# Performance work log

Hardware: AMD Instinct MI355X
Metric: run time of the kernel (lower is better)

The kernel has to match this reference:

```python
import jax, jax.numpy as jnp
import numpy as np

N_OUT = 100_000   # destination (output) nodes
N_IN = 200_000    # source nodes (x_feat rows); first N_OUT are the self/dst nodes
DEG = 16          # sample_count / fixed fan-out
E = N_OUT * DEG   # edges
D_IN = 128
D_OUT = 128


def setup_inputs() -> dict:
    key = jax.random.key(0)
    k1, k2, k3 = jax.random.split(key, 3)
    x_feat = jax.random.normal(k1, (N_IN, D_IN), dtype=jnp.float32)
    # MFG CSR with fixed fan-out DEG (what make_mfg_csr(sample_size=DEG) encodes)
    csr_row_ptr = jnp.arange(N_OUT + 1, dtype=jnp.int64) * DEG
    csr_col_ind = jax.random.randint(k2, (E,), 0, N_IN, dtype=jnp.int64)
    # Linear(2*D_IN, D_OUT) with xavier_uniform(gain for relu) weight
    gain = float(np.sqrt(2.0))
    fan_in, fan_out = 2 * D_IN, D_OUT
    bound = gain * float(np.sqrt(6.0 / (fan_in + fan_out)))
    W = jax.random.uniform(k3, (D_OUT, 2 * D_IN), dtype=jnp.float32,
                           minval=-bound, maxval=bound)
    lin_bias = jnp.zeros((D_OUT,), dtype=jnp.float32)
    bias = jnp.zeros((D_OUT,), dtype=jnp.float32)  # extra additive Parameter
    return {"x_feat": x_feat, "csr_row_ptr": csr_row_ptr,
            "csr_col_ind": csr_col_ind, "sample_count": DEG,
            "W": W, "lin_bias": lin_bias, "bias": bias}


def _segment_ids(row_ptr, n_edges):
    # seg[e] = destination row of edge e; handles empty rows via duplicate adds
    ones = jnp.zeros((n_edges,), dtype=jnp.int32).at[row_ptr[1:-1]].add(1)
    return jnp.cumsum(ones)


def reference(x_feat, csr_row_ptr, csr_col_ind, sample_count, W, lin_bias, bias):
    n_out = csr_row_ptr.shape[0] - 1
    n_edges = csr_col_ind.shape[0]
    seg = _segment_ids(csr_row_ptr, n_edges)
    # mean aggregation over sampled neighbors (cugraphops agg 'mean')
    gathered = x_feat[csr_col_ind]                          # [E, D_IN]
    summed = jax.ops.segment_sum(gathered, seg, num_segments=n_out)
    deg = (csr_row_ptr[1:] - csr_row_ptr[:-1]).astype(x_feat.dtype)
    mean_agg = summed / jnp.maximum(deg, 1.0)[:, None]      # [n_out, D_IN]
    # concat self (dst) features with aggregated features, then Linear
    x_agg = jnp.concatenate([x_feat[:n_out], mean_agg], axis=-1)  # [n_out, 2*D_IN]
    y = x_agg @ W.T + lin_bias + bias
    return y
```

## Files before the change

kernel.cpp:

```cpp
#include <hip/hip_runtime.h>
#include <hip/hip_bf16.h>

#define D 128
#define K2 256
#define NT 64
#define NTHREADS 256
#define AGM_LD 136
#define WT_LD 68

typedef __attribute__((ext_vector_type(8))) short bf16x8;
typedef __attribute__((ext_vector_type(4))) float f32x4;
typedef __attribute__((ext_vector_type(2))) float f32x2;

static __device__ __forceinline__ unsigned short f2bf(float f) {
    __hip_bfloat16 h = __float2bfloat16(f);
    return *reinterpret_cast<unsigned short*>(&h);
}

static __device__ __forceinline__ unsigned int f2q_manual(float f) {
    f = fminf(fmaxf(f, -448.f), 448.f);
    unsigned int u = __float_as_uint(f * 0x1.0p-120f);
    const unsigned int lsb = (u >> 20) & 1u;
    u += 0x7ffffu + lsb;
    return ((u >> 24) & 0x80u) | ((u >> 20) & 0x7fu);
}
static __device__ __forceinline__ float q2f_manual(unsigned int b) {
    const unsigned int bits = ((b & 0x80u) << 24) | ((b & 0x7fu) << 20);
    return __uint_as_float(bits) * 0x1.0p+120f;
}
static __device__ __forceinline__ unsigned int pack_fp8x4(float4 v) {
#if __has_builtin(__builtin_amdgcn_cvt_pk_fp8_f32)
    int lo = __builtin_amdgcn_cvt_pk_fp8_f32(v.x, v.y, 0, false);
    int q  = __builtin_amdgcn_cvt_pk_fp8_f32(v.z, v.w, lo, true);
    return (unsigned int)q;
#else
    return f2q_manual(v.x) | (f2q_manual(v.y) << 8) |
           (f2q_manual(v.z) << 16) | (f2q_manual(v.w) << 24);
#endif
}
static __device__ __forceinline__ f32x2 unpack_fp8_lo(unsigned int v) {
#if __has_builtin(__builtin_amdgcn_cvt_pk_f32_fp8)
    return __builtin_amdgcn_cvt_pk_f32_fp8((int)v, false);
#else
    f32x2 r; r[0] = q2f_manual(v & 0xffu); r[1] = q2f_manual((v >> 8) & 0xffu); return r;
#endif
}
static __device__ __forceinline__ f32x2 unpack_fp8_hi(unsigned int v) {
#if __has_builtin(__builtin_amdgcn_cvt_pk_f32_fp8)
    return __builtin_amdgcn_cvt_pk_f32_fp8((int)v, true);
#else
    f32x2 r; r[0] = q2f_manual((v >> 16) & 0xffu); r[1] = q2f_manual((v >> 24) & 0xffu); return r;
#endif
}

__global__ __launch_bounds__(256)
void convert_all(const float* __restrict__ x, const float* __restrict__ W,
                 unsigned int* __restrict__ xq4,
                 uint2* __restrict__ xbs4,
                 uint2* __restrict__ wb4,
                 long n4x, long n4s, long n4w)
{
    const long gid = (long)blockIdx.x * blockDim.x + threadIdx.x;
    const long stride = (long)gridDim.x * blockDim.x;
    for (long t = gid; t < n4x; t += stride) {
        const float4 v = reinterpret_cast<const float4*>(x)[t];
        xq4[t] = pack_fp8x4(v);
        if (t < n4s) {
            uint2 p;
            p.x = (unsigned int)f2bf(v.x) | ((unsigned int)f2bf(v.y) << 16);
            p.y = (unsigned int)f2bf(v.z) | ((unsigned int)f2bf(v.w) << 16);
            xbs4[t] = p;
        }
    }
    for (long t = gid; t < n4w; t += stride) {
        const float4 v = reinterpret_cast<const float4*>(W)[t];
        uint2 p;
        p.x = (unsigned int)f2bf(v.x) | ((unsigned int)f2bf(v.y) << 16);
        p.y = (unsigned int)f2bf(v.z) | ((unsigned int)f2bf(v.w) << 16);
        wb4[t] = p;
    }
}

__global__ __launch_bounds__(NTHREADS, 4)
void sage_fp8b(const unsigned char* __restrict__ xq,
               const unsigned short* __restrict__ xbs,
               const unsigned short* __restrict__ wb,
               const int* __restrict__ rp,
               const int* __restrict__ ci,
               const float* __restrict__ lb,
               const float* __restrict__ bb,
               float* __restrict__ y,
               int n_out)
{
    __shared__ unsigned short aggM[NT][AGM_LD];
    __shared__ unsigned short wtT[D][WT_LD];
    __shared__ int rpls[NT + 1];
    __shared__ int cils[NT * 16];

    const int tid   = threadIdx.x;
    const int wave  = tid >> 6;
    const int lane  = tid & 63;
    const int node0 = blockIdx.x * NT;
    const int nt_act = min(NT, n_out - node0);

    if (tid <= nt_act) rpls[tid] = rp[node0 + tid];
    __syncthreads();
    const int e_base = rpls[0];
    const int e_cnt  = rpls[nt_act] - e_base;
    const bool fits  = (e_cnt <= NT * 16);
    if (fits) {
        for (int i = tid; i < e_cnt; i += NTHREADS) cils[i] = ci[e_base + i];
    }
    __syncthreads();

    const int nsel = lane >> 5;
    const int dg4  = (lane & 31) * 4;

    for (int p = 0; p < 8; ++p) {
        const int n0 = wave * 16 + p * 2;
        if (n0 >= nt_act) break;
        const bool has1 = (n0 + 1 < nt_act);

        const int s0 = rpls[n0] - e_base;
        const int d0 = rpls[n0 + 1] - e_base - s0;
        int s1 = s0, d1 = d0;
        if (has1) { s1 = rpls[n0 + 1] - e_base; d1 = rpls[n0 + 2] - e_base - s1; }

        const int  my_n   = n0 + nsel;
        const int  my_s   = nsel ? s1 : s0;
        const int  my_d   = nsel ? d1 : d0;
        const bool active = (nsel == 0) || has1;

        float a0 = 0.f, a1 = 0.f, a2 = 0.f, a3 = 0.f;
        if (fits && has1 && d0 == 16 && d1 == 16) {
            int idx[16];
            #pragma unroll
            for (int u = 0; u < 16; ++u) idx[u] = cils[my_s + u];
            #pragma unroll
            for (int u = 0; u < 16; ++u) {
                const unsigned int v = *reinterpret_cast<const unsigned int*>(
                    &xq[(size_t)idx[u] * D + dg4]);
                const f32x2 lo = unpack_fp8_lo(v);
                const f32x2 hi = unpack_fp8_hi(v);
                a0 += lo[0]; a1 += lo[1]; a2 += hi[0]; a3 += hi[1];
            }
        } else if (active) {
            for (int u = 0; u < my_d; ++u) {
                const int c = fits ? cils[my_s + u] : ci[e_base + my_s + u];
                const unsigned int v = *reinterpret_cast<const unsigned int*>(
                    &xq[(size_t)c * D + dg4]);
                const f32x2 lo = unpack_fp8_lo(v);
                const f32x2 hi = unpack_fp8_hi(v);
                a0 += lo[0]; a1 += lo[1]; a2 += hi[0]; a3 += hi[1];
            }
        }
        if (active) {
            const float inv = 1.0f / (float)max(my_d, 1);
            uint2 pk;
            pk.x = (unsigned int)f2bf(a0 * inv) | ((unsigned int)f2bf(a1 * inv) << 16);
            pk.y = (unsigned int)f2bf(a2 * inv) | ((unsigned int)f2bf(a3 * inv) << 16);
            *reinterpret_cast<uint2*>(&aggM[my_n][dg4]) = pk;
        }
    }

    const int n15 = lane & 15;
    const int g   = lane >> 4;

    const int arow = min(node0 + wave * 16 + n15, n_out - 1);
    bf16x8 aself[4];
    #pragma unroll
    for (int c = 0; c < 4; ++c)
        aself[c] = *reinterpret_cast<const bf16x8*>(
            &xbs[(size_t)arow * D + c * 32 + g * 8]);

    f32x4 acc[8];
    #pragma unroll
    for (int f = 0; f < 8; ++f) acc[f] = (f32x4){0.f, 0.f, 0.f, 0.f};

    #pragma unroll
    for (int ch = 0; ch < 4; ++ch) {
        const int k0 = ch * 64;
        #pragma unroll
        for (int j = 0; j < 8; ++j) {
            const int flat = j * 256 + tid;
            const int o    = flat >> 4;
            const int q    = flat & 15;
            *reinterpret_cast<uint2*>(&wtT[o][q * 4]) =
                *reinterpret_cast<const uint2*>(&wb[(size_t)o * K2 + k0 + q * 4]);
        }
        __syncthreads();

        #pragma unroll
        for (int sub = 0; sub < 2; ++sub) {
            const int kk = k0 + sub * 32;
            const bf16x8 a = (kk < 128)
                ? aself[ch * 2 + sub]
                : *reinterpret_cast<const bf16x8*>(
                      &aggM[wave * 16 + n15][(kk - 128) + g * 8]);
            #pragma unroll
            for (int f = 0; f < 8; ++f) {
                const bf16x8 b = *reinterpret_cast<const bf16x8*>(
                    &wtT[f * 16 + n15][sub * 32 + g * 8]);
                acc[f] = __builtin_amdgcn_mfma_f32_16x16x32_bf16(a, b, acc[f], 0, 0, 0);
            }
        }
        __syncthreads();
    }

    const int mbase = node0 + wave * 16 + g * 4;
    #pragma unroll
    for (int f = 0; f < 8; ++f) {
        const int col  = f * 16 + n15;
        const float bs = lb[col] + bb[col];
        #pragma unroll
        for (int r = 0; r < 4; ++r) {
            const int row = mbase + r;
            if (row < n_out)
                y[(size_t)row * D + col] = acc[f][r] + bs;
        }
    }
}

#define AGG_LDF 264
__global__ __launch_bounds__(NTHREADS, 3)
void sage_fused3(const float* __restrict__ x,
                 const int* __restrict__ rp,
                 const int* __restrict__ ci,
                 const float* __restrict__ W,
                 const float* __restrict__ lb,
                 const float* __restrict__ bb,
                 float* __restrict__ y,
                 int n_out)
{
    __shared__ unsigned short aggB[NT][AGG_LDF];
    __shared__ unsigned short wtTF[D][32];
    __shared__ int rpls[NT + 1];
    __shared__ int cilsF[NT * 16];

    const int tid   = threadIdx.x;
    const int wave  = tid >> 6;
    const int lane  = tid & 63;
    const int node0 = blockIdx.x * NT;
    const int nt_act = min(NT, n_out - node0);

    if (tid <= nt_act) rpls[tid] = rp[node0 + tid];
    __syncthreads();
    const int e_base = rpls[0];
    const int e_cnt  = rpls[nt_act] - e_base;
    const bool fits  = (e_cnt <= NT * 16);
    if (fits) {
        for (int i = tid; i < e_cnt; i += NTHREADS) cilsF[i] = ci[e_base + i];
    }
    __syncthreads();

    for (int t = 0; t < 16; ++t) {
        const int nn = wave * 16 + t;
        if (nn >= nt_act) break;
        const int node = node0 + nn;
        const float2 self =
            *reinterpret_cast<const float2*>(&x[(size_t)node * D + lane * 2]);
        const int s  = rpls[nn] - e_base;
        const int dg = rpls[nn + 1] - e_base - s;
        float ax = 0.f, ay = 0.f;
        for (int u = 0; u < dg; ++u) {
            const int c = fits ? cilsF[s + u] : ci[e_base + s + u];
            const float2 v = *reinterpret_cast<const float2*>(
                &x[(size_t)c * D + lane * 2]);
            ax += v.x; ay += v.y;
        }
        const float inv = 1.0f / (float)max(dg, 1);
        *reinterpret_cast<unsigned int*>(&aggB[nn][lane * 2]) =
            (unsigned int)f2bf(self.x) | ((unsigned int)f2bf(self.y) << 16);
        *reinterpret_cast<unsigned int*>(&aggB[nn][D + lane * 2]) =
            (unsigned int)f2bf(ax * inv) | ((unsigned int)f2bf(ay * inv) << 16);
    }

    const int n15 = lane & 15;
    const int g   = lane >> 4;
    f32x4 acc[8];
    #pragma unroll
    for (int f = 0; f < 8; ++f) acc[f] = (f32x4){0.f, 0.f, 0.f, 0.f};

    for (int k0 = 0; k0 < K2; k0 += 32) {
        #pragma unroll
        for (int j = 0; j < 4; ++j) {
            const int idx = j * 256 + tid;
            const int o   = idx >> 3;
            const int c   = idx & 7;
            const float4 w = *reinterpret_cast<const float4*>(
                &W[(size_t)o * K2 + k0 + c * 4]);
            const unsigned int lo = (unsigned int)f2bf(w.x) | ((unsigned int)f2bf(w.y) << 16);
            const unsigned int hi = (unsigned int)f2bf(w.z) | ((unsigned int)f2bf(w.w) << 16);
            *reinterpret_cast<uint2*>(&wtTF[o][c * 4]) = make_uint2(lo, hi);
        }
        __syncthreads();
        const bf16x8 a = *reinterpret_cast<const bf16x8*>(
            &aggB[wave * 16 + n15][k0 + g * 8]);
        #pragma unroll
        for (int f = 0; f < 8; ++f) {
            const bf16x8 b = *reinterpret_cast<const bf16x8*>(&wtTF[f * 16 + n15][g * 8]);
            acc[f] = __builtin_amdgcn_mfma_f32_16x16x32_bf16(a, b, acc[f], 0, 0, 0);
        }
        __syncthreads();
    }

    const int mbase = node0 + wave * 16 + g * 4;
    #pragma unroll
    for (int f = 0; f < 8; ++f) {
        const int col  = f * 16 + n15;
        const float bs = lb[col] + bb[col];
        #pragma unroll
        for (int r = 0; r < 4; ++r) {
            const int row = mbase + r;
            if (row < n_out)
                y[(size_t)row * D + col] = acc[f][r] + bs;
        }
    }
}

extern "C" void kernel_launch(void* const* d_in, const int* in_sizes, int n_in,
                              void* d_out, int out_size, void* d_ws, size_t ws_size,
                              hipStream_t stream)
{
    const float* x  = (const float*)d_in[0];
    const int*   rp = (const int*)d_in[1];
    const int*   ci = (const int*)d_in[2];
    const float* W  = (const float*)d_in[4];
    const float* lb = (const float*)d_in[5];
    const float* bb = (const float*)d_in[6];
    float* y = (float*)d_out;

    const int n_out = in_sizes[1] - 1;
    const int grid  = (n_out + NT - 1) / NT;

    const size_t n_x = (size_t)in_sizes[0];
    const size_t n_w = (size_t)in_sizes[4];
    const size_t xq_bytes  = n_x;
    const size_t xbs_bytes = (size_t)n_out * D * 2;
    const size_t wb_bytes  = n_w * 2;
    const size_t need = xq_bytes + xbs_bytes + wb_bytes;

    if (ws_size >= need) {
        unsigned char*  xq  = (unsigned char*)d_ws;
        unsigned short* xbs = (unsigned short*)((char*)d_ws + xq_bytes);
        unsigned short* wb  = (unsigned short*)((char*)d_ws + xq_bytes + xbs_bytes);
        hipLaunchKernelGGL(convert_all, dim3(2048), dim3(256), 0, stream,
                           x, W, (unsigned int*)xq, (uint2*)xbs, (uint2*)wb,
                           (long)(n_x >> 2), (long)(((size_t)n_out * D) >> 2),
                           (long)(n_w >> 2));
        hipLaunchKernelGGL(sage_fp8b, dim3(grid), dim3(NTHREADS), 0, stream,
                           xq, xbs, wb, rp, ci, lb, bb, y, n_out);
    } else {
        hipLaunchKernelGGL(sage_fused3, dim3(grid), dim3(NTHREADS), 0, stream,
                           x, rp, ci, W, lb, bb, y, n_out);
    }
}
```

Before: 78.93 us.

## Widen fp8 gathers to 8 bytes and stage output through shared memory

The aggregation loop now handles four nodes per wave, with each lane loading 8 fp8 values (uint2) instead of 4, so fewer but wider gather loads are issued per row. The MFMA accumulators are written into a shared-memory tile that aliases the aggM/wtT buffers. The tile is then read back row-major so global stores of y become coalesced float4 writes instead of scattered scalar stores. This trades extra LDS traffic and a fast-path condition that needs a wave vote for better global store and gather efficiency. The aliasing relies on all waves finishing their MFMA reads before any wave writes the tile.

```diff
diff --git a/kernel.cpp b/kernel.cpp
--- a/kernel.cpp
+++ b/kernel.cpp
@@ -7,6 +7,7 @@
 #define NTHREADS 256
 #define AGM_LD 136
 #define WT_LD 68
+#define YT_LD 129
 
 typedef __attribute__((ext_vector_type(8))) short bf16x8;
 typedef __attribute__((ext_vector_type(4))) float f32x4;
@@ -82,7 +83,7 @@
 }
 
 __global__ __launch_bounds__(NTHREADS, 4)
-void sage_fp8b(const unsigned char* __restrict__ xq,
+void sage_fp8c(const unsigned char* __restrict__ xq,
                const unsigned short* __restrict__ xbs,
                const unsigned short* __restrict__ wb,
                const int* __restrict__ rp,
@@ -92,8 +93,10 @@
                float* __restrict__ y,
                int n_out)
 {
-    __shared__ unsigned short aggM[NT][AGM_LD];
-    __shared__ unsigned short wtT[D][WT_LD];
+    __shared__ __align__(16) unsigned char smraw[34816];
+    auto aggM  = reinterpret_cast<unsigned short (*)[AGM_LD]>(smraw);
+    auto wtT   = reinterpret_cast<unsigned short (*)[WT_LD]>(smraw + 17408);
+    auto ytile = reinterpret_cast<float (*)[YT_LD]>(smraw);
     __shared__ int rpls[NT + 1];
     __shared__ int cils[NT * 16];
 
@@ -113,53 +116,60 @@
     }
     __syncthreads();
 
-    const int nsel = lane >> 5;
-    const int dg4  = (lane & 31) * 4;
-
-    for (int p = 0; p < 8; ++p) {
-        const int n0 = wave * 16 + p * 2;
+    const int nsel = lane >> 4;
+    const int dl   = (lane & 15) * 8;
+
+    for (int p = 0; p < 4; ++p) {
+        const int n0 = wave * 16 + p * 4;
         if (n0 >= nt_act) break;
-        const bool has1 = (n0 + 1 < nt_act);
-
-        const int s0 = rpls[n0] - e_base;
-        const int d0 = rpls[n0 + 1] - e_base - s0;
-        int s1 = s0, d1 = d0;
-        if (has1) { s1 = rpls[n0 + 1] - e_base; d1 = rpls[n0 + 2] - e_base - s1; }
-
-        const int  my_n   = n0 + nsel;
-        const int  my_s   = nsel ? s1 : s0;
-        const int  my_d   = nsel ? d1 : d0;
-        const bool active = (nsel == 0) || has1;
-
-        float a0 = 0.f, a1 = 0.f, a2 = 0.f, a3 = 0.f;
-        if (fits && has1 && d0 == 16 && d1 == 16) {
+        const int nrem   = nt_act - n0;
+        const int my_n   = n0 + nsel;
+        const bool active = (nsel < nrem);
+
+        int my_s = 0, my_d = 0;
+        if (active) {
+            my_s = rpls[my_n] - e_base;
+            my_d = rpls[my_n + 1] - e_base - my_s;
+        }
+
+        float a0=0.f,a1=0.f,a2=0.f,a3=0.f,a4=0.f,a5=0.f,a6=0.f,a7=0.f;
+        const bool fast = fits && (nrem >= 4) && __all(my_d == 16);
+        if (fast) {
             int idx[16];
             #pragma unroll
             for (int u = 0; u < 16; ++u) idx[u] = cils[my_s + u];
             #pragma unroll
             for (int u = 0; u < 16; ++u) {
-                const unsigned int v = *reinterpret_cast<const unsigned int*>(
-                    &xq[(size_t)idx[u] * D + dg4]);
-                const f32x2 lo = unpack_fp8_lo(v);
-                const f32x2 hi = unpack_fp8_hi(v);
-                a0 += lo[0]; a1 += lo[1]; a2 += hi[0]; a3 += hi[1];
+                const uint2 v = *reinterpret_cast<const uint2*>(
+                    &xq[(size_t)idx[u] * D + dl]);
+                const f32x2 e0 = unpack_fp8_lo(v.x);
+                const f32x2 e1 = unpack_fp8_hi(v.x);
+                const f32x2 e2 = unpack_fp8_lo(v.y);
+                const f32x2 e3 = unpack_fp8_hi(v.y);
+                a0 += e0[0]; a1 += e0[1]; a2 += e1[0]; a3 += e1[1];
+                a4 += e2[0]; a5 += e2[1]; a6 += e3[0]; a7 += e3[1];
             }
         } else if (active) {
             for (int u = 0; u < my_d; ++u) {
                 const int c = fits ? cils[my_s + u] : ci[e_base + my_s + u];
-                const unsigned int v = *reinterpret_cast<const unsigned int*>(
-                    &xq[(size_t)c * D + dg4]);
-                const f32x2 lo = unpack_fp8_lo(v);
-                const f32x2 hi = unpack_fp8_hi(v);
-                a0 += lo[0]; a1 += lo[1]; a2 += hi[0]; a3 += hi[1];
+                const uint2 v = *reinterpret_cast<const uint2*>(
+                    &xq[(size_t)c * D + dl]);
+                const f32x2 e0 = unpack_fp8_lo(v.x);
+                const f32x2 e1 = unpack_fp8_hi(v.x);
+                const f32x2 e2 = unpack_fp8_lo(v.y);
+                const f32x2 e3 = unpack_fp8_hi(v.y);
+                a0 += e0[0]; a1 += e0[1]; a2 += e1[0]; a3 += e1[1];
+                a4 += e2[0]; a5 += e2[1]; a6 += e3[0]; a7 += e3[1];
             }
         }
         if (active) {
             const float inv = 1.0f / (float)max(my_d, 1);
-            uint2 pk;
+            uint4 pk;
             pk.x = (unsigned int)f2bf(a0 * inv) | ((unsigned int)f2bf(a1 * inv) << 16);
             pk.y = (unsigned int)f2bf(a2 * inv) | ((unsigned int)f2bf(a3 * inv) << 16);
-            *reinterpret_cast<uint2*>(&aggM[my_n][dg4]) = pk;
+            pk.z = (unsigned int)f2bf(a4 * inv) | ((unsigned int)f2bf(a5 * inv) << 16);
+            pk.w = (unsigned int)f2bf(a6 * inv) | ((unsigned int)f2bf(a7 * inv) << 16);
+            *reinterpret_cast<uint4*>(&aggM[my_n][dl]) = pk;
         }
     }
 
@@ -207,17 +217,27 @@
         __syncthreads();
     }
 
-    const int mbase = node0 + wave * 16 + g * 4;
     #pragma unroll
     for (int f = 0; f < 8; ++f) {
-        const int col  = f * 16 + n15;
-        const float bs = lb[col] + bb[col];
-        #pragma unroll
-        for (int r = 0; r < 4; ++r) {
-            const int row = mbase + r;
-            if (row < n_out)
-                y[(size_t)row * D + col] = acc[f][r] + bs;
-        }
+        #pragma unroll
+        for (int r = 0; r < 4; ++r)
+            ytile[wave * 16 + g * 4 + r][f * 16 + n15] = acc[f][r];
+    }
+
+    const int c4 = (lane & 31) * 4;
+    const float4 blv = *reinterpret_cast<const float4*>(&lb[c4]);
+    const float4 bbv = *reinterpret_cast<const float4*>(&bb[c4]);
+    const float bx = blv.x + bbv.x, by = blv.y + bbv.y;
+    const float bz = blv.z + bbv.z, bw = blv.w + bbv.w;
+
+    #pragma unroll
+    for (int pass = 0; pass < 8; ++pass) {
+        const int rl  = pass * 2 + (lane >> 5);
+        const int row = node0 + wave * 16 + rl;
+        float4 v = *reinterpret_cast<const float4*>(&ytile[wave * 16 + rl][c4]);
+        v.x += bx; v.y += by; v.z += bz; v.w += bw;
+        if (row < n_out)
+            *reinterpret_cast<float4*>(&y[(size_t)row * D + c4]) = v;
     }
 }
 
@@ -234,7 +254,7 @@
 {
     __shared__ unsigned short aggB[NT][AGG_LDF];
     __shared__ unsigned short wtTF[D][32];
-    __shared__ int rpls[NT + 1];
+    __shared__ int rplsF[NT + 1];
     __shared__ int cilsF[NT * 16];
 
     const int tid   = threadIdx.x;
@@ -243,10 +263,10 @@
     const int node0 = blockIdx.x * NT;
     const int nt_act = min(NT, n_out - node0);
 
-    if (tid <= nt_act) rpls[tid] = rp[node0 + tid];
+    if (tid <= nt_act) rplsF[tid] = rp[node0 + tid];
     __syncthreads();
-    const int e_base = rpls[0];
-    const int e_cnt  = rpls[nt_act] - e_base;
+    const int e_base = rplsF[0];
+    const int e_cnt  = rplsF[nt_act] - e_base;
     const bool fits  = (e_cnt <= NT * 16);
     if (fits) {
         for (int i = tid; i < e_cnt; i += NTHREADS) cilsF[i] = ci[e_base + i];
@@ -259,8 +279,8 @@
         const int node = node0 + nn;
         const float2 self =
             *reinterpret_cast<const float2*>(&x[(size_t)node * D + lane * 2]);
-        const int s  = rpls[nn] - e_base;
-        const int dg = rpls[nn + 1] - e_base - s;
+        const int s  = rplsF[nn] - e_base;
+        const int dg = rplsF[nn + 1] - e_base - s;
         float ax = 0.f, ay = 0.f;
         for (int u = 0; u < dg; ++u) {
             const int c = fits ? cilsF[s + u] : ci[e_base + s + u];
@@ -348,7 +368,7 @@
                            x, W, (unsigned int*)xq, (uint2*)xbs, (uint2*)wb,
                            (long)(n_x >> 2), (long)(((size_t)n_out * D) >> 2),
                            (long)(n_w >> 2));
-        hipLaunchKernelGGL(sage_fp8b, dim3(grid), dim3(NTHREADS), 0, stream,
+        hipLaunchKernelGGL(sage_fp8c, dim3(grid), dim3(NTHREADS), 0, stream,
                            xq, xbs, wb, rp, ci, lb, bb, y, n_out);
     } else {
         hipLaunchKernelGGL(sage_fused3, dim3(grid), dim3(NTHREADS), 0, stream,
```

Result: slower. 107.5 us (+36.2%).
